# Performance work log

Hardware: AMD Instinct MI355X
Metric: run time of the kernel (lower is better)

The kernel has to match this reference:

```python
import jax, jax.numpy as jnp
import numpy as np

N_LAYER, N_HEAD, N_EMBD, VOCAB, T_CTX, MAXT, B = 6, 8, 128, 18, 30, 2719, 64


def _ln(x, g, b, eps=1e-5):
    m = x.mean(-1, keepdims=True)
    v = ((x - m) ** 2).mean(-1, keepdims=True)
    return (x - m) * jax.lax.rsqrt(v + eps) * g + b


def setup_inputs() -> dict:
    key = jax.random.key(0)
    ks = iter(jax.random.split(key, 64))
    nrm = lambda shape: jax.random.normal(next(ks), shape, jnp.float32) * 0.02
    E, L4 = N_EMBD, 4 * N_EMBD
    inp = dict(
        states=jax.random.normal(next(ks), (B, T_CTX, 4, 84, 84), jnp.float32),
        actions=jax.random.randint(next(ks), (B, T_CTX, 1), 0, VOCAB),
        rtgs=jax.random.normal(next(ks), (B, T_CTX, 1), jnp.float32),
        timesteps=jax.random.randint(next(ks), (B, 1, 1), 0, MAXT),
        conv_w=nrm((E, 4, 84, 84)),
        class_tok=nrm((1, 1, E)),
        in_proj_w=nrm((3 * E, E)), in_proj_b=jnp.zeros(3 * E),
        out_w=nrm((E, E)), out_b=jnp.zeros(E),
        iln1_g=jnp.ones(E), iln1_b=jnp.zeros(E),
        iln2_g=jnp.ones(E), iln2_b=jnp.zeros(E),
        ffn_w1=nrm((E, E)), ffn_b1=jnp.zeros(E),
        ffn_w2=nrm((E, E)), ffn_b2=jnp.zeros(E),
        ret_w=nrm((E, 1)), ret_b=jnp.zeros(E),
        act_table=nrm((VOCAB, E)),
        pos_emb=nrm((1, 3 * T_CTX + 1, E)),
        global_pos_emb=nrm((1, MAXT + 1, E)),
        ln1_g=jnp.ones((N_LAYER, E)), ln1_b=jnp.zeros((N_LAYER, E)),
        Wq=nrm((N_LAYER, E, E)), bq=jnp.zeros((N_LAYER, E)),
        Wk=nrm((N_LAYER, E, E)), bk=jnp.zeros((N_LAYER, E)),
        Wv=nrm((N_LAYER, E, E)), bv=jnp.zeros((N_LAYER, E)),
        Wo=nrm((N_LAYER, E, E)), bo=jnp.zeros((N_LAYER, E)),
        ln2_g=jnp.ones((N_LAYER, E)), ln2_b=jnp.zeros((N_LAYER, E)),
        W1=nrm((N_LAYER, L4, E)), b1=jnp.zeros((N_LAYER, L4)),
        W2=nrm((N_LAYER, E, L4)), b2=jnp.zeros((N_LAYER, E)),
        lnf_g=jnp.ones(E), lnf_b=jnp.zeros(E),
        head_w=nrm((VOCAB, E)),
    )
    return inp


def _forward(states, actions, rtgs, timesteps, conv_w, class_tok, in_proj_w, in_proj_b,
             out_w, out_b, iln1_g, iln1_b, iln2_g, iln2_b, ffn_w1, ffn_b1, ffn_w2, ffn_b2,
             ret_w, ret_b, act_table, pos_emb, global_pos_emb,
             ln1_g, ln1_b, Wq, bq, Wk, bk, Wv, bv, Wo, bo, ln2_g, ln2_b,
             W1, b1, W2, b2, lnf_g, lnf_b, head_w):
    Bsz, T = states.shape[:2]
    E = conv_w.shape[0]
    H, hd = N_HEAD, E // N_HEAD
    # --- inner TIT: patch embed (kernel 84 = frame size -> single patch = one big dot) ---
    obs = states.reshape(Bsz * T, *states.shape[2:])                      # (BT,4,84,84)
    patch = jnp.einsum('bchw,echw->be', obs, conv_w)[:, None, :]          # (BT,1,E)
    x = jnp.concatenate([jnp.broadcast_to(class_tok, (Bsz * T, 1, E)), patch], axis=1)  # (BT,2,E)
    h = _ln(x, iln1_g, iln1_b)
    q, k, v = jnp.split(h @ in_proj_w.T + in_proj_b, 3, axis=-1)
    att = jax.nn.softmax(jnp.einsum('bqe,bke->bqk', q, k) / jnp.sqrt(jnp.float32(E)), axis=-1)
    x = x + jnp.einsum('bqk,bke->bqe', att, v) @ out_w.T + out_b
    h2 = _ln(x, iln2_g, iln2_b)
    x = x + jax.nn.relu(h2 @ ffn_w1.T + ffn_b1) @ ffn_w2.T + ffn_b2
    state_emb = x[:, 0, :].reshape(Bsz, T, E)                             # class token
    # --- token interleave (targets=None path -> length 3T-1, last T-1 actions) ---
    rtg_emb = jnp.tanh(rtgs @ ret_w.T + ret_b)                            # (B,T,E)
    act_emb = jnp.tanh(act_table[actions[..., 0]])                        # (B,T,E)
    Lt = 3 * T - 1
    tok = jnp.zeros((Bsz, Lt, E), states.dtype)
    tok = tok.at[:, 0::3].set(rtg_emb).at[:, 1::3].set(state_emb).at[:, 2::3].set(act_emb[:, 1:])
    pos = global_pos_emb[0][timesteps[:, 0, 0]][:, None, :] + pos_emb[:, :Lt, :]
    x = tok + pos
    # --- outer causal GPT blocks ---
    mask = jnp.tril(jnp.ones((Lt, Lt), bool))
    for i in range(N_LAYER):
        hh = _ln(x, ln1_g[i], ln1_b[i])
        proj = lambda w, b: (hh @ w.T + b).reshape(Bsz, Lt, H, hd).transpose(0, 2, 1, 3)
        q, k, v = proj(Wq[i], bq[i]), proj(Wk[i], bk[i]), proj(Wv[i], bv[i])
        att = jnp.einsum('bhqd,bhkd->bhqk', q, k) / jnp.sqrt(jnp.float32(hd))
        att = jax.nn.softmax(jnp.where(mask, att, -jnp.inf), axis=-1)
        y = jnp.einsum('bhqk,bhkd->bhqd', att, v).transpose(0, 2, 1, 3).reshape(Bsz, Lt, E)
        x = x + y @ Wo[i].T + bo[i]
        hh2 = _ln(x, ln2_g[i], ln2_b[i])
        x = x + jax.nn.gelu(hh2 @ W1[i].T + b1[i], approximate=False) @ W2[i].T + b2[i]
    logits = _ln(x, lnf_g, lnf_b) @ head_w.T
    return logits[:, 1::3, :]                                             # (B,T,vocab) state-position logits


def reference(states, actions, rtgs, timesteps, conv_w, class_tok, in_proj_w, in_proj_b,
              out_w, out_b, iln1_g, iln1_b, iln2_g, iln2_b, ffn_w1, ffn_b1, ffn_w2, ffn_b2,
              ret_w, ret_b, act_table, pos_emb, global_pos_emb,
              ln1_g, ln1_b, Wq, bq, Wk, bk, Wv, bv, Wo, bo, ln2_g, ln2_b,
              W1, b1, W2, b2, lnf_g, lnf_b, head_w):
    return _forward(states, actions, rtgs, timesteps, conv_w, class_tok, in_proj_w, in_proj_b,
                    out_w, out_b, iln1_g, iln1_b, iln2_g, iln2_b, ffn_w1, ffn_b1, ffn_w2, ffn_b2,
                    ret_w, ret_b, act_table, pos_emb, global_pos_emb,
                    ln1_g, ln1_b, Wq, bq, Wk, bk, Wv, bv, Wo, bo, ln2_g, ln2_b,
                    W1, b1, W2, b2, lnf_g, lnf_b, head_w)
```

## Files before the change

### kernel.cpp

```cpp
#include <hip/hip_runtime.h>

#define NB   64
#define NT   30
#define NBT  1920
#define EE   128
#define KP   28224
#define LTK  89
#define NS   5696
#define NLY  6
#define NV   18
#define NZ   21

typedef unsigned short ushort_t;
using bf16x8 = __attribute__((ext_vector_type(8))) short;
using us8    = __attribute__((ext_vector_type(8))) unsigned short;
using f32x4  = __attribute__((ext_vector_type(4))) float;
using f32x16 = __attribute__((ext_vector_type(16))) float;

__device__ inline ushort_t f2bf(float f){
  union { float f; unsigned u; } v; v.f = f;
  unsigned r = v.u + 0x7FFFu + ((v.u >> 16) & 1u);
  return (ushort_t)(r >> 16);
}
__device__ inline float bf2f(ushort_t h){
  union { unsigned u; float f; } v; v.u = ((unsigned)h) << 16; return v.f;
}

__global__ __launch_bounds__(256) void wcvt(
  const float* conv, const float* Wq, const float* Wk, const float* Wv,
  const float* Wo, const float* W1, const float* W2,
  const float* in_w, const float* out_w, const float* f1w, const float* f2w,
  const float* bq, const float* bk, const float* bv,
  ushort_t* dc, ushort_t* dqkv, ushort_t* dout, ushort_t* d1, ushort_t* d2,
  ushort_t* dinw, ushort_t* doutw, ushort_t* df1, ushort_t* df2, float* bqkv)
{
  if (blockIdx.x >= 4776){
    int idx = (blockIdx.x-4776)*256 + threadIdx.x;
    if (idx < NLY*128){ int l=idx>>7, j=idx&127;
      bqkv[l*384+j]=bq[idx]; bqkv[l*384+128+j]=bk[idx]; bqkv[l*384+256+j]=bv[idx]; }
    return;
  }
  long i = 4l*((long)blockIdx.x*256 + threadIdx.x);
  if (i >= 3612672l && i < 3907584l){
    long o = i - 3612672l;
    int  seg = (int)(o / 98304l);
    long off2 = o - (long)seg*98304l;
    long layer = off2 >> 14, rem = off2 & 16383l;
    const float* s = (seg==0) ? Wq : (seg==1) ? Wk : Wv;
    float4 f = *reinterpret_cast<const float4*>(s+off2);
    long dst = layer*49152l + (long)seg*16384l + rem;
    dqkv[dst]=f2bf(f.x); dqkv[dst+1]=f2bf(f.y); dqkv[dst+2]=f2bf(f.z); dqkv[dst+3]=f2bf(f.w);
    return;
  }
  const float* s; ushort_t* d; long off;
  if      (i < 3612672l){ s=conv;  d=dc;    off=i; }
  else if (i < 4005888l){ s=Wo;    d=dout;  off=i-3907584l; }
  else if (i < 4399104l){ s=W1;    d=d1;    off=i-4005888l; }
  else if (i < 4792320l){ s=W2;    d=d2;    off=i-4399104l; }
  else if (i < 4841472l){ s=in_w;  d=dinw;  off=i-4792320l; }
  else if (i < 4857856l){ s=out_w; d=doutw; off=i-4841472l; }
  else if (i < 4874240l){ s=f1w;   d=df1;   off=i-4857856l; }
  else                  { s=f2w;   d=df2;   off=i-4874240l; }
  float4 f = *reinterpret_cast<const float4*>(s+off);
  d[off]=f2bf(f.x); d[off+1]=f2bf(f.y); d[off+2]=f2bf(f.z); d[off+3]=f2bf(f.w);
}

__global__ __launch_bounds__(256) void patch_gemm(
  const float* __restrict__ A, const ushort_t* __restrict__ Wb, float* __restrict__ C)
{
  __shared__ __align__(16) ushort_t As[2][64*64];
  __shared__ __align__(16) ushort_t Ws[2][128*64];
  const int tid = threadIdx.x, lane = tid & 63, wid = tid >> 6;
  const int m0 = blockIdx.x * 64;
  const int kbase = blockIdx.z * 1344;
  float* Cz = C + (size_t)blockIdx.z * NBT * EE;
  const int ra = tid>>2, ca = (tid&3)*16, swa = (ra&7)<<3;
  const int rw = tid>>1, cw = (tid&1)*32, sww = (rw&7)<<3;
  const float*    Ab = A  + (size_t)(m0+ra)*KP + kbase + ca;
  const ushort_t* Wp = Wb + (size_t)rw*KP  + kbase + cw;
  f32x4 acc[8];
  #pragma unroll
  for (int j=0;j<8;j++) acc[j] = (f32x4){0.f,0.f,0.f,0.f};

  auto loadT = [&](float4 (&fa)[4], us8 (&wr)[4], int kt){
    #pragma unroll
    for (int q=0;q<4;q++){
      fa[q] = *reinterpret_cast<const float4*>(Ab + kt*64 + 4*q);
      wr[q] = *reinterpret_cast<const us8*>(Wp + kt*64 + 8*q);
    }
  };
  auto commitT = [&](int buf, const float4 (&fa)[4], const us8 (&wr)[4]){
    us8 o0, o1;
    o0[0]=f2bf(fa[0].x); o0[1]=f2bf(fa[0].y); o0[2]=f2bf(fa[0].z); o0[3]=f2bf(fa[0].w);
    o0[4]=f2bf(fa[1].x); o0[5]=f2bf(fa[1].y); o0[6]=f2bf(fa[1].z); o0[7]=f2bf(fa[1].w);
    o1[0]=f2bf(fa[2].x); o1[1]=f2bf(fa[2].y); o1[2]=f2bf(fa[2].z); o1[3]=f2bf(fa[2].w);
    o1[4]=f2bf(fa[3].x); o1[5]=f2bf(fa[3].y); o1[6]=f2bf(fa[3].z); o1[7]=f2bf(fa[3].w);
    *reinterpret_cast<us8*>(&As[buf][ra*64 + ( ca    ^ swa)]) = o0;
    *reinterpret_cast<us8*>(&As[buf][ra*64 + ((ca+8) ^ swa)]) = o1;
    #pragma unroll
    for (int q=0;q<4;q++)
      *reinterpret_cast<us8*>(&Ws[buf][rw*64 + ((cw+8*q) ^ sww)]) = wr[q];
  };
  auto computeT = [&](int buf){
    #pragma unroll
    for (int ks=0; ks<2; ++ks){
      int arow = wid*16 + (lane&15);
      int kb = ks*32 + (lane>>4)*8;
      bf16x8 a = *reinterpret_cast<const bf16x8*>(&As[buf][arow*64 + (kb ^ ((arow&7)<<3))]);
      #pragma unroll
      for (int nt=0; nt<8; ++nt){
        int nn = nt*16 + (lane&15);
        bf16x8 b = *reinterpret_cast<const bf16x8*>(&Ws[buf][nn*64 + (kb ^ ((nn&7)<<3))]);
        acc[nt] = __builtin_amdgcn_mfma_f32_16x16x32_bf16(a, b, acc[nt], 0,0,0);
      }
    }
  };

  float4 faA[4], faB[4]; us8 wrA[4], wrB[4];
  loadT(faA, wrA, 0);
  loadT(faB, wrB, 1);
  for (int kp = 0; kp < 11; ++kp){
    int kt0 = 2*kp;
    commitT(0, faA, wrA);
    if (kt0 + 2 < 21) loadT(faA, wrA, kt0 + 2);
    __syncthreads();
    computeT(0);
    int kt1 = kt0 + 1;
    if (kt1 < 21){
      commitT(1, faB, wrB);
      if (kt1 + 2 < 21) loadT(faB, wrB, kt1 + 2);
      __syncthreads();
      computeT(1);
    }
  }
  #pragma unroll
  for (int nt=0; nt<8; ++nt)
    #pragma unroll
    for (int rr=0;rr<4;rr++){
      int row = m0 + wid*16 + (lane>>4)*4 + rr;
      int col = nt*16 + (lane&15);
      Cz[row*EE + col] = acc[nt][rr];
    }
}

__global__ __launch_bounds__(256, 2) void inner_tit(
  const float* __restrict__ part, const float* __restrict__ ctok,
  const ushort_t* __restrict__ inw, const float* __restrict__ in_b,
  const ushort_t* __restrict__ outw, const float* __restrict__ out_b,
  const float* __restrict__ g1, const float* __restrict__ b1_,
  const float* __restrict__ g2, const float* __restrict__ b2_,
  const ushort_t* __restrict__ f1wb, const float* __restrict__ fb1,
  const ushort_t* __restrict__ f2wb, const float* __restrict__ fb2,
  const float* __restrict__ rtgs, const int* __restrict__ actions,
  const int* __restrict__ tsteps, const float* __restrict__ ret_w,
  const float* __restrict__ ret_b, const float* __restrict__ act_tab,
  const float* __restrict__ pos_emb, const float* __restrict__ gpos,
  const float* __restrict__ ln1g0, const float* __restrict__ ln1b0,
  float* __restrict__ x, ushort_t* __restrict__ xln)
{
  __shared__ __align__(16) ushort_t wbuf[192*128];
  __shared__ float xs[16*128];
  __shared__ __align__(16) ushort_t hb[16*128];
  __shared__ __align__(16) ushort_t hf[16*128];
  __shared__ __align__(16) ushort_t qkvb[16*400];
  __shared__ float ssm[32];
  const int tid = threadIdx.x, lane = tid & 63, wid = tid >> 6;
  const int bt0 = blockIdx.x * 8;

  auto stageWB = [&](const ushort_t* src, int R){
    for (int c = tid; c < R*16; c += 256){
      int rr = c >> 4, cc = (c & 15) * 8;
      *reinterpret_cast<us8*>(&wbuf[rr*128 + (cc ^ ((rr&7)<<3))]) =
        *reinterpret_cast<const us8*>(src + (size_t)rr*128 + cc);
    }
  };
  auto lnrow = [&](const float* gam, const float* bet, ushort_t* dst){
    int r = tid >> 4, e0 = (tid & 15) * 8;
    float v[8];
    #pragma unroll
    for (int j=0;j<8;j++) v[j] = xs[r*128 + e0 + j];
    float s = 0;
    #pragma unroll
    for (int j=0;j<8;j++) s += v[j];
    s += __shfl_xor(s,1); s += __shfl_xor(s,2); s += __shfl_xor(s,4); s += __shfl_xor(s,8);
    float mean = s * (1.0f/128.0f);
    float vs = 0;
    #pragma unroll
    for (int j=0;j<8;j++){ float d = v[j]-mean; vs += d*d; }
    vs += __shfl_xor(vs,1); vs += __shfl_xor(vs,2); vs += __shfl_xor(vs,4); vs += __shfl_xor(vs,8);
    float rstd = rsqrtf(vs*(1.0f/128.0f) + 1e-5f);
    us8 o;
    #pragma unroll
    for (int j=0;j<8;j++) o[j] = f2bf((v[j]-mean)*rstd*gam[e0+j] + bet[e0+j]);
    *reinterpret_cast<us8*>(&dst[r*128 + (e0 ^ ((r&7)<<3))]) = o;
  };
  auto qgemm = [&](const ushort_t* abuf, int ntg, int rowoff, f32x4& acc){
    int al = lane & 15, kq = (lane>>4)*8;
    int nrow = (ntg*16 + al) - rowoff, nsw = (nrow&7)<<3;
    #pragma unroll
    for (int ks=0; ks<4; ++ks){
      int kb = ks*32 + kq;
      bf16x8 a = *reinterpret_cast<const bf16x8*>(&abuf[al*128 + (kb ^ ((al&7)<<3))]);
      bf16x8 b = *reinterpret_cast<const bf16x8*>(&wbuf[nrow*128 + (kb ^ nsw)]);
      acc = __builtin_amdgcn_mfma_f32_16x16x32_bf16(a, b, acc, 0,0,0);
    }
  };

  { int r = tid >> 4, e0 = (tid & 15) * 8;
    float v[8];
    if ((r & 1) == 0){
      #pragma unroll
      for (int j=0;j<8;j++) v[j] = ctok[e0+j];
    } else {
      #pragma unroll
      for (int j=0;j<8;j++) v[j] = 0.f;
      int bt = bt0 + (r>>1);
      for (int z=0; z<NZ; ++z){
        const float* p = part + (size_t)z*NBT*EE + (size_t)bt*128 + e0;
        float4 f0 = *reinterpret_cast<const float4*>(p);
        float4 f1 = *reinterpret_cast<const float4*>(p+4);
        v[0]+=f0.x; v[1]+=f0.y; v[2]+=f0.z; v[3]+=f0.w;
        v[4]+=f1.x; v[5]+=f1.y; v[6]+=f1.z; v[7]+=f1.w;
      }
    }
    #pragma unroll
    for (int j=0;j<8;j++) xs[r*128 + e0 + j] = v[j];
  }
  stageWB(inw, 192);
  __syncthreads();

  lnrow(g1, b1_, hb);
  __syncthreads();

  { int al = lane & 15;
    #pragma unroll
    for (int j=0;j<3;++j){
      int nt = wid*3 + j;
      f32x4 acc = (f32x4){0.f,0.f,0.f,0.f};
      qgemm(hb, nt, 0, acc);
      float bia = in_b[nt*16 + al];
      #pragma unroll
      for (int rr=0; rr<4; ++rr){
        int row = (lane>>4)*4 + rr;
        qkvb[row*400 + nt*16 + al] = f2bf(acc[rr] + bia);
      }
    }
  }
  __syncthreads();
  stageWB(inw + (size_t)192*128, 192);
  __syncthreads();
  { int al = lane & 15;
    #pragma unroll
    for (int j=0;j<3;++j){
      int nt = 12 + wid*3 + j;
      f32x4 acc = (f32x4){0.f,0.f,0.f,0.f};
      qgemm(hb, nt, 192, acc);
      float bia = in_b[nt*16 + al];
      #pragma unroll
      for (int rr=0; rr<4; ++rr){
        int row = (lane>>4)*4 + rr;
        qkvb[row*400 + nt*16 + al] = f2bf(acc[rr] + bia);
      }
    }
  }
  __syncthreads();

  { int d = tid >> 3, j = tid & 7;
    int i = d >> 2, p = d & 3;
    const ushort_t* qp = &qkvb[(2*i + (p>>1))*400 + j*16];
    const ushort_t* kp = &qkvb[(2*i + (p&1))*400 + 128 + j*16];
    float s = 0;
    #pragma unroll
    for (int e=0;e<16;e++) s += bf2f(qp[e])*bf2f(kp[e]);
    s += __shfl_xor(s,1); s += __shfl_xor(s,2); s += __shfl_xor(s,4);
    if (j == 0) ssm[d] = s;
  }
  stageWB(outw, 128);
  __syncthreads();

  { int r = tid >> 4, e0 = (tid & 15)*8;
    int i = r >> 1, t = r & 1;
    const float sc = 0.08838834764831845f;
    float s0 = ssm[i*4 + t*2]*sc, s1 = ssm[i*4 + t*2 + 1]*sc;
    float m = fmaxf(s0,s1), p0 = __expf(s0-m), p1 = __expf(s1-m);
    float iv = 1.0f/(p0+p1); p0 *= iv; p1 *= iv;
    const ushort_t* v0 = &qkvb[(2*i)*400 + 256 + e0];
    const ushort_t* v1 = &qkvb[(2*i+1)*400 + 256 + e0];
    us8 o;
    #pragma unroll
    for (int j=0;j<8;j++) o[j] = f2bf(p0*bf2f(v0[j]) + p1*bf2f(v1[j]));
    *reinterpret_cast<us8*>(&hb[r*128 + (e0 ^ ((r&7)<<3))]) = o;
  }
  __syncthreads();

  { int al = lane & 15;
    #pragma unroll
    for (int j=0;j<2;++j){
      int nt = wid*2 + j;
      f32x4 acc = (f32x4){0.f,0.f,0.f,0.f};
      qgemm(hb, nt, 0, acc);
      float bia = out_b[nt*16 + al];
      #pragma unroll
      for (int rr=0; rr<4; ++rr){
        int row = (lane>>4)*4 + rr;
        xs[row*128 + nt*16 + al] += acc[rr] + bia;
      }
    }
  }
  __syncthreads();

  lnrow(g2, b2_, hb);
  stageWB(f1wb, 128);
  __syncthreads();

  { int al = lane & 15;
    #pragma unroll
    for (int j=0;j<2;++j){
      int nt = wid*2 + j;
      f32x4 acc = (f32x4){0.f,0.f,0.f,0.f};
      qgemm(hb, nt, 0, acc);
      float bia = fb1[nt*16 + al];
      #pragma unroll
      for (int rr=0; rr<4; ++rr){
        int row = (lane>>4)*4 + rr;
        hf[row*128 + ((nt*16+al) ^ ((row&7)<<3))] = f2bf(fmaxf(acc[rr] + bia, 0.f));
      }
    }
  }
  __syncthreads();

  stageWB(f2wb, 128);
  __syncthreads();
  { int al = lane & 15;
    #pragma unroll
    for (int j=0;j<2;++j){
      int nt = wid*2 + j;
      f32x4 acc = (f32x4){0.f,0.f,0.f,0.f};
      qgemm(hf, nt, 0, acc);
      float bia = fb2[nt*16 + al];
      #pragma unroll
      for (int rr=0; rr<4; ++rr){
        int row = (lane>>4)*4 + rr;
        xs[row*128 + nt*16 + al] += acc[rr] + bia;
      }
    }
  }
  __syncthreads();

  { int q = tid >> 3, j = tid & 7;
    if (q < 24){
      int i = q / 3, kind = q - 3*i;
      int btg = bt0 + i, b = btg / NT, t = btg - b*NT;
      bool valid = !(kind == 2 && t == 0);
      if (valid){
        int prow = (kind==0) ? 3*t : (kind==1) ? 3*t+1 : 3*t-1;
        size_t xrow = ((size_t)b*LTK + prow)*128;
        int ts = tsteps[b];
        int e0 = j*16;
        float v[16];
        if (kind == 1){
          #pragma unroll
          for (int e=0;e<16;e++) v[e] = xs[(2*i)*128 + e0 + e];
        } else if (kind == 0){
          float rv = rtgs[b*NT+t];
          #pragma unroll
          for (int e=0;e<16;e++) v[e] = tanhf(rv*ret_w[e0+e] + ret_b[e0+e]);
        } else {
          int a = actions[b*NT+t];
          #pragma unroll
          for (int e=0;e<16;e++) v[e] = tanhf(act_tab[a*128 + e0 + e]);
        }
        #pragma unroll
        for (int e=0;e<16;e++)
          v[e] += gpos[(size_t)ts*128 + e0 + e] + pos_emb[prow*128 + e0 + e];
        #pragma unroll
        for (int e=0;e<16;e++) x[xrow + e0 + e] = v[e];
        float s = 0;
        #pragma unroll
        for (int e=0;e<16;e++) s += v[e];
        s += __shfl_xor(s,1); s += __shfl_xor(s,2); s += __shfl_xor(s,4);
        float mean = s * (1.0f/128.0f);
        float vs = 0;
        #pragma unroll
        for (int e=0;e<16;e++){ float d = v[e]-mean; vs += d*d; }
        vs += __shfl_xor(vs,1); vs += __shfl_xor(vs,2); vs += __shfl_xor(vs,4);
        float rstd = rsqrtf(vs*(1.0f/128.0f) + 1e-5f);
        #pragma unroll
        for (int e=0;e<16;e++)
          xln[xrow + e0 + e] = f2bf((v[e]-mean)*rstd*ln1g0[e0+e] + ln1b0[e0+e]);
      }
    }
  }
}

__global__ __launch_bounds__(256, 2) void attn_fused(
  const ushort_t* __restrict__ xln, const ushort_t* __restrict__ Wqkv,
  const float* __restrict__ bqkv, ushort_t* __restrict__ y)
{
  __shared__ __align__(16) char sm[69504];
  ushort_t* ab  = (ushort_t*)sm;
  ushort_t* wb  = (ushort_t*)(sm + 24576);
  float*    S   = (float*)sm;
  ushort_t* qa  = (ushort_t*)(sm + 37248);
  ushort_t* ka  = (ushort_t*)(sm + 41472);
  ushort_t* vta = (ushort_t*)(sm + 45696);
  ushort_t* pb  = (ushort_t*)(sm + 49152);
  float*    inv = (float*)(sm + 69120);

  const int b = blockIdx.x >> 3, h = blockIdx.x & 7;
  const int tid = threadIdx.x, lane = tid & 63, wid = tid >> 6;

  for (int idx = tid; idx < 1536; idx += 256){
    int row = idx >> 4, c0 = (idx & 15) * 8;
    us8 v;
    if (row < LTK) v = *reinterpret_cast<const us8*>(xln + ((size_t)(b*LTK+row))*128 + c0);
    else           v = (us8){0,0,0,0,0,0,0,0};
    *reinterpret_cast<us8*>(&ab[row*128 + (c0 ^ ((row&7)<<3))]) = v;
  }
  for (int idx = tid; idx < 384; idx += 256){
    int rr = idx >> 3, c = (idx & 7) * 16;
    int seg = rr >> 4, n = rr & 15;
    const ushort_t* src = Wqkv + (size_t)(seg*128 + h*16 + n)*128 + c;
    int sw = (rr&7)<<3;
    *reinterpret_cast<us8*>(&wb[rr*128 + ( c    ^ sw)]) = *reinterpret_cast<const us8*>(src);
    *reinterpret_cast<us8*>(&wb[rr*128 + ((c+8) ^ sw)]) = *reinterpret_cast<const us8*>(src+8);
  }
  __syncthreads();

  for (int idx = wid; idx < 18; idx += 4){
    int rt = idx / 3, nt = idx - 3*(idx/3);
    f32x4 acc = (f32x4){0.f,0.f,0.f,0.f};
    int arow = rt*16 + (lane&15), asw = (arow&7)<<3;
    int nrow = nt*16 + (lane&15), nsw = (nrow&7)<<3;
    #pragma unroll
    for (int ks=0; ks<4; ++ks){
      int kb = ks*32 + (lane>>4)*8;
      bf16x8 a = *reinterpret_cast<const bf16x8*>(&ab[arow*128 + (kb ^ asw)]);
      bf16x8 bf = *reinterpret_cast<const bf16x8*>(&wb[nrow*128 + (kb ^ nsw)]);
      acc = __builtin_amdgcn_mfma_f32_16x16x32_bf16(a, bf, acc, 0,0,0);
    }
    int d = lane & 15;
    float bia = bqkv[nt*128 + h*16 + d];
    #pragma unroll
    for (int rr=0; rr<4; ++rr){
      int rg = rt*16 + (lane>>4)*4 + rr;
      ushort_t hv = f2bf(acc[rr] + bia);
      if      (nt == 0) qa[rg*22 + d] = hv;
      else if (nt == 1) ka[rg*22 + d] = hv;
      else              vta[d*108 + rg] = hv;
    }
  }
  __syncthreads();

  {
    static const int TR[6] = {0,1,1,2,2,2};
    static const int TC[6] = {0,0,1,0,1,2};
    for (int idx = wid; idx < 6; idx += 4){
      int R = TR[idx], C = TC[idx];
      int arow = R*32 + (lane&31), brow = C*32 + (lane&31);
      int ke = (lane>>5)*8;
      bf16x8 a  = *reinterpret_cast<const bf16x8*>(&qa[arow*22 + ke]);
      bf16x8 bf = *reinterpret_cast<const bf16x8*>(&ka[brow*22 + ke]);
      f32x16 sc = {};
      sc = __builtin_amdgcn_mfma_f32_32x32x16_bf16(a, bf, sc, 0,0,0);
      #pragma unroll
      for (int r=0; r<16; ++r){
        int rin = (r&3) + 8*(r>>2) + 4*(lane>>5);
        S[(R*32+rin)*97 + C*32 + (lane&31)] = sc[r]*0.25f;
      }
    }
  }
  __syncthreads();

  if (tid < 192){
    int t = tid >> 1, half = tid & 1;
    int u0 = half*48;
    float mx = -1e30f;
    if (t < LTK){
      for (int u=u0; u<u0+48; ++u) if (u<=t) mx = fmaxf(mx, S[t*97+u]);
    }
    mx = fmaxf(mx, __shfl_xor(mx,1));
    float smv = 0;
    if (t < LTK){
      for (int u=u0; u<u0+48; ++u){
        float p = 0;
        if (u<=t){ p = __expf(S[t*97+u]-mx); smv += p; }
        pb[t*104+u] = f2bf(p);
      }
    } else {
      for (int u=u0; u<u0+48; ++u) pb[t*104+u] = 0;
    }
    smv += __shfl_xor(smv,1);
    if (half==0) inv[t] = (t<LTK) ? 1.0f/smv : 0.0f;
  }
  __syncthreads();

  for (int rt = wid; rt < 6; rt += 4){
    int arow = rt*16 + (lane&15);
    f32x4 acc = (f32x4){0.f,0.f,0.f,0.f};
    #pragma unroll
    for (int ks=0; ks<3; ++ks){
      int kb = ks*32 + (lane>>4)*8;
      bf16x8 a  = *reinterpret_cast<const bf16x8*>(&pb[arow*104 + kb]);
      bf16x8 bf = *reinterpret_cast<const bf16x8*>(&vta[(lane&15)*108 + kb]);
      acc = __builtin_amdgcn_mfma_f32_16x16x32_bf16(a, bf, acc, 0,0,0);
    }
    #pragma unroll
    for (int rr=0; rr<4; ++rr){
      int rg = rt*16 + (lane>>4)*4 + rr;
      if (rg < LTK)
        y[(size_t)(b*LTK+rg)*128 + h*16 + (lane&15)] = f2bf(acc[rr]*inv[rg]);
    }
  }
}

template<bool HEAD>
__global__ __launch_bounds__(256, 2) void ffn_fused(
  const ushort_t* __restrict__ yg, const ushort_t* __restrict__ Wo,
  const float* __restrict__ bo, const float* __restrict__ g2,
  const float* __restrict__ b2g, const ushort_t* __restrict__ W1,
  const float* __restrict__ b1v, const ushort_t* __restrict__ W2,
  const float* __restrict__ b2v, float* __restrict__ x,
  const float* __restrict__ lnng, const float* __restrict__ lnnb,
  ushort_t* __restrict__ xlnout,
  const float* __restrict__ lnfg, const float* __restrict__ lnfb,
  const float* __restrict__ hw, float* __restrict__ out)
{
  __shared__ __align__(16) char sm[66304];
  ushort_t* wdb = (ushort_t*)sm;
  float*    xr  = (float*)(sm + 32768);
  ushort_t* h2  = (ushort_t*)(sm + 49664);
  ushort_t* f1  = (ushort_t*)(sm + 57856);
  const int tid = threadIdx.x, lane = tid & 63, wid = tid >> 6;
  const int m0 = blockIdx.x * 32;
  const int rr = tid >> 2, qq = tid & 3, swr = (rr&7)<<3;

  auto srcp = [&](int s)->const ushort_t* {
    if (s == 0) return Wo + (size_t)rr*128 + qq*32;
    if (s == 1) return Wo + (size_t)(64+rr)*128 + qq*32;
    int c = (s-2)>>2, r = (s-2)&3;
    if (r == 0) return W1 + (size_t)(c*128+rr)*128 + qq*32;
    if (r == 1) return W1 + (size_t)(c*128+64+rr)*128 + qq*32;
    if (r == 2) return W2 + (size_t)rr*512 + c*128 + qq*32;
    return W2 + (size_t)(64+rr)*512 + c*128 + qq*32;
  };
  auto issue = [&](us8 (&r)[4], int s){
    const ushort_t* p = srcp(s);
    #pragma unroll
    for (int g=0; g<4; ++g) r[g] = *reinterpret_cast<const us8*>(p + 8*g);
  };
  auto commit = [&](int buf, const us8 (&r)[4]){
    ushort_t* d = wdb + buf*8192 + rr*128;
    #pragma unroll
    for (int g=0; g<4; ++g)
      *reinterpret_cast<us8*>(&d[(qq*32+8*g) ^ swr]) = r[g];
  };
  auto gemmT = [&](const ushort_t* abuf, int buf, f32x4* accp){
    int nrow = wid*16 + (lane&15), nsw = (nrow&7)<<3;
    #pragma unroll
    for (int rt=0; rt<2; ++rt){
      int arow = rt*16 + (lane&15), asw = (arow&7)<<3;
      #pragma unroll
      for (int ks=0; ks<4; ++ks){
        int kb = ks*32 + (lane>>4)*8;
        bf16x8 a  = *reinterpret_cast<const bf16x8*>(&abuf[arow*128 + (kb ^ asw)]);
        bf16x8 bb = *reinterpret_cast<const bf16x8*>(&wdb[buf*8192 + nrow*128 + (kb ^ nsw)]);
        accp[rt] = __builtin_amdgcn_mfma_f32_16x16x32_bf16(a, bb, accp[rt], 0,0,0);
      }
    }
  };

  f32x4 accA[2][2], acc2[2][2];
  #pragma unroll
  for (int s_=0;s_<2;++s_){
    accA[s_][0]=(f32x4){0,0,0,0}; accA[s_][1]=(f32x4){0,0,0,0};
    acc2[s_][0]=(f32x4){0,0,0,0}; acc2[s_][1]=(f32x4){0,0,0,0};
  }

  auto computeStage = [&](int k, int buf){
    if (k == 0){
      gemmT(f1, buf, accA[0]);
    } else if (k == 1){
      gemmT(f1, buf, accA[1]);
      #pragma unroll
      for (int s_=0; s_<2; ++s_){
        int col = s_*64 + wid*16 + (lane&15);
        float bia = bo[col];
        #pragma unroll
        for (int rt=0; rt<2; ++rt)
          #pragma unroll
          for (int r4=0; r4<4; ++r4){
            int row = rt*16 + (lane>>4)*4 + r4;
            xr[row*132 + col] = accA[s_][rt][r4] + bia + x[(size_t)(m0+row)*128 + col];
          }
      }
      __syncthreads();
      { int r8 = tid>>3, q8 = tid&7;
        float xv[16];
        #pragma unroll
        for (int i=0;i<16;i++) xv[i] = xr[r8*132 + q8*16 + i];
        float s = 0;
        #pragma unroll
        for (int i=0;i<16;i++) s += xv[i];
        s += __shfl_xor(s,1); s += __shfl_xor(s,2); s += __shfl_xor(s,4);
        float mean = s * (1.0f/128.0f);
        float vs = 0;
        #pragma unroll
        for (int i=0;i<16;i++){ float d = xv[i]-mean; vs += d*d; }
        vs += __shfl_xor(vs,1); vs += __shfl_xor(vs,2); vs += __shfl_xor(vs,4);
        float rstd = rsqrtf(vs*(1.0f/128.0f) + 1e-5f);
        int sw = (r8&7)<<3;
        #pragma unroll
        for (int g=0; g<2; ++g){
          us8 o;
          #pragma unroll
          for (int jj=0;jj<8;jj++){
            int c = q8*16 + g*8 + jj;
            o[jj] = f2bf((xv[g*8+jj]-mean)*rstd*g2[c] + b2g[c]);
          }
          *reinterpret_cast<us8*>(&h2[r8*128 + ((q8*16+g*8) ^ sw)]) = o;
        }
      }
    } else {
      int r = (k-2)&3, c = (k-2)>>2;
      if (r < 2){
        f32x4 ac[2] = {(f32x4){0,0,0,0},(f32x4){0,0,0,0}};
        gemmT(h2, buf, ac);
        int cl = r*64 + wid*16 + (lane&15);
        float bia = b1v[c*128 + cl];
        #pragma unroll
        for (int rt=0; rt<2; ++rt)
          #pragma unroll
          for (int r4=0; r4<4; ++r4){
            int row = rt*16 + (lane>>4)*4 + r4;
            float v = ac[rt][r4] + bia;
            v = 0.5f*v*(1.0f + erff(v*0.70710678118654752f));
            f1[row*128 + (cl ^ ((row&7)<<3))] = f2bf(v);
          }
      } else if (r == 2){
        gemmT(f1, buf, acc2[0]);
      } else {
        gemmT(f1, buf, acc2[1]);
      }
    }
  };

  { int r8 = tid>>3, q8 = tid&7, sw = (r8&7)<<3;
    const ushort_t* src = yg + (size_t)(m0+r8)*128 + q8*16;
    *reinterpret_cast<us8*>(&f1[r8*128 + ((q8*16)   ^ sw)]) = *reinterpret_cast<const us8*>(src);
    *reinterpret_cast<us8*>(&f1[r8*128 + ((q8*16+8) ^ sw)]) = *reinterpret_cast<const us8*>(src+8);
  }
  us8 rA[4], rB[4];
  issue(rA, 0); issue(rB, 1);

  for (int kp = 0; kp < 9; ++kp){
    int k0 = 2*kp, k1 = 2*kp + 1;
    commit(0, rA);
    if (k0 + 2 < 18) issue(rA, k0 + 2);
    __syncthreads();
    computeStage(k0, 0);
    commit(1, rB);
    if (k1 + 2 < 18) issue(rB, k1 + 2);
    __syncthreads();
    computeStage(k1, 1);
  }

  #pragma unroll
  for (int s_=0; s_<2; ++s_){
    int col = s_*64 + wid*16 + (lane&15);
    float bia = b2v[col];
    #pragma unroll
    for (int rt=0; rt<2; ++rt)
      #pragma unroll
      for (int r4=0; r4<4; ++r4){
        int row = rt*16 + (lane>>4)*4 + r4;
        float v = acc2[s_][rt][r4] + bia + xr[row*132 + col];
        xr[row*132 + col] = v;
        if constexpr (!HEAD) x[(size_t)(m0+row)*128 + col] = v;
      }
  }
  __syncthreads();
  if constexpr (!HEAD){
    int r8 = tid>>3, q8 = tid&7;
    float xv[16];
    #pragma unroll
    for (int i=0;i<16;i++) xv[i] = xr[r8*132 + q8*16 + i];
    float s = 0;
    #pragma unroll
    for (int i=0;i<16;i++) s += xv[i];
    s += __shfl_xor(s,1); s += __shfl_xor(s,2); s += __shfl_xor(s,4);
    float mean = s * (1.0f/128.0f);
    float vs = 0;
    #pragma unroll
    for (int i=0;i<16;i++){ float d = xv[i]-mean; vs += d*d; }
    vs += __shfl_xor(vs,1); vs += __shfl_xor(vs,2); vs += __shfl_xor(vs,4);
    float rstd = rsqrtf(vs*(1.0f/128.0f) + 1e-5f);
    #pragma unroll
    for (int g=0; g<2; ++g){
      us8 o;
      #pragma unroll
      for (int jj=0;jj<8;jj++){
        int c = q8*16 + g*8 + jj;
        o[jj] = f2bf((xv[g*8+jj]-mean)*rstd*lnng[c] + lnnb[c]);
      }
      *reinterpret_cast<us8*>(xlnout + (size_t)(m0+r8)*128 + q8*16 + g*8) = o;
    }
  } else {
    for (int r = wid; r < 32; r += 4){
      int s = m0 + r, bb2 = s / LTK, p = s - bb2*LTK;
      if (p % 3 != 1) continue;
      int t = p / 3;
      float v1 = xr[r*132 + lane];
      float v2 = xr[r*132 + 64 + lane];
      float sum = v1 + v2;
      sum += __shfl_xor(sum,1); sum += __shfl_xor(sum,2); sum += __shfl_xor(sum,4);
      sum += __shfl_xor(sum,8); sum += __shfl_xor(sum,16); sum += __shfl_xor(sum,32);
      float mean = sum*(1.0f/128.0f);
      float d1 = v1-mean, d2 = v2-mean;
      float var = d1*d1 + d2*d2;
      var += __shfl_xor(var,1); var += __shfl_xor(var,2); var += __shfl_xor(var,4);
      var += __shfl_xor(var,8); var += __shfl_xor(var,16); var += __shfl_xor(var,32);
      float rstd = rsqrtf(var*(1.0f/128.0f) + 1e-5f);
      float h1 = d1*rstd*lnfg[lane]    + lnfb[lane];
      float h2v= d2*rstd*lnfg[lane+64] + lnfb[lane+64];
      #pragma unroll
      for (int o=0; o<NV; ++o){
        float sdot = h1*hw[o*128+lane] + h2v*hw[o*128+lane+64];
        sdot += __shfl_xor(sdot,1); sdot += __shfl_xor(sdot,2); sdot += __shfl_xor(sdot,4);
        sdot += __shfl_xor(sdot,8); sdot += __shfl_xor(sdot,16); sdot += __shfl_xor(sdot,32);
        if (lane == 0) out[(size_t)(bb2*NT+t)*NV + o] = sdot;
      }
    }
  }
}

extern "C" void kernel_launch(void* const* d_in, const int* in_sizes, int n_in,
                              void* d_out, int out_size, void* d_ws, size_t ws_size,
                              hipStream_t stream)
{
  const float* states  = (const float*)d_in[0];
  const int*   actions = (const int*)  d_in[1];
  const float* rtgs    = (const float*)d_in[2];
  const int*   tsteps  = (const int*)  d_in[3];
  const float* conv_w  = (const float*)d_in[4];
  const float* ctok    = (const float*)d_in[5];
  const float* in_w    = (const float*)d_in[6];
  const float* in_b    = (const float*)d_in[7];
  const float* out_w   = (const float*)d_in[8];
  const float* out_b   = (const float*)d_in[9];
  const float* i1g     = (const float*)d_in[10];
  const float* i1b     = (const float*)d_in[11];
  const float* i2g     = (const float*)d_in[12];
  const float* i2b     = (const float*)d_in[13];
  const float* fw1     = (const float*)d_in[14];
  const float* fb1     = (const float*)d_in[15];
  const float* fw2     = (const float*)d_in[16];
  const float* fb2     = (const float*)d_in[17];
  const float* ret_w   = (const float*)d_in[18];
  const float* ret_b   = (const float*)d_in[19];
  const float* act_tab = (const float*)d_in[20];
  const float* pos_emb = (const float*)d_in[21];
  const float* gpos    = (const float*)d_in[22];
  const float* ln1g    = (const float*)d_in[23];
  const float* ln1b    = (const float*)d_in[24];
  const float* Wq      = (const float*)d_in[25];
  const float* bq      = (const float*)d_in[26];
  const float* Wk      = (const float*)d_in[27];
  const float* bk      = (const float*)d_in[28];
  const float* Wv      = (const float*)d_in[29];
  const float* bv      = (const float*)d_in[30];
  const float* Wo      = (const float*)d_in[31];
  const float* bo      = (const float*)d_in[32];
  const float* ln2g    = (const float*)d_in[33];
  const float* ln2b    = (const float*)d_in[34];
  const float* W1      = (const float*)d_in[35];
  const float* b1      = (const float*)d_in[36];
  const float* W2      = (const float*)d_in[37];
  const float* b2      = (const float*)d_in[38];
  const float* lnfg    = (const float*)d_in[39];
  const float* lnfb    = (const float*)d_in[40];
  const float* head_w  = (const float*)d_in[41];

  char* w = (char*)d_ws;
  size_t off = 0;
  auto alloc = [&](size_t bytes)->char* {
    char* p = w + off; off += (bytes + 255) & ~(size_t)255; return p;
  };
  float*    part  = (float*)   alloc((size_t)NZ*NBT*EE*4);
  float*    x     = (float*)   alloc((size_t)NS*EE*4);
  ushort_t* xlnA  = (ushort_t*)alloc((size_t)NS*EE*2);
  ushort_t* xlnB  = (ushort_t*)alloc((size_t)NS*EE*2);
  ushort_t* yb    = (ushort_t*)alloc((size_t)NS*EE*2);
  ushort_t* cwb   = (ushort_t*)alloc((size_t)EE*KP*2);
  ushort_t* Wqkvb = (ushort_t*)alloc((size_t)NLY*384*128*2);
  ushort_t* Wob   = (ushort_t*)alloc((size_t)NLY*128*128*2);
  ushort_t* W1b   = (ushort_t*)alloc((size_t)NLY*512*128*2);
  ushort_t* W2b   = (ushort_t*)alloc((size_t)NLY*128*512*2);
  ushort_t* inwb  = (ushort_t*)alloc((size_t)384*128*2);
  ushort_t* outwb = (ushort_t*)alloc((size_t)128*128*2);
  ushort_t* f1wb  = (ushort_t*)alloc((size_t)128*128*2);
  ushort_t* f2wb  = (ushort_t*)alloc((size_t)128*128*2);
  float*    bqkv  = (float*)   alloc(NLY*384*4);
  (void)in_sizes; (void)n_in; (void)out_size; (void)ws_size;

  wcvt<<<4779,256,0,stream>>>(conv_w,Wq,Wk,Wv,Wo,W1,W2,
                              in_w,out_w,fw1,fw2, bq,bk,bv,
                              cwb,Wqkvb,Wob,W1b,W2b,
                              inwb,outwb,f1wb,f2wb, bqkv);
  patch_gemm<<<dim3(30,1,NZ),256,0,stream>>>(states, cwb, part);
  inner_tit<<<240,256,0,stream>>>(part, ctok, inwb, in_b, outwb, out_b,
                                  i1g,i1b,i2g,i2b, f1wb,fb1, f2wb,fb2,
                                  rtgs, actions, tsteps, ret_w, ret_b, act_tab,
                                  pos_emb, gpos, ln1g, ln1b, x, xlnA);
  for (int i=0;i<NLY;i++){
    ushort_t* xin  = (i & 1) ? xlnB : xlnA;
    ushort_t* xout = (i & 1) ? xlnA : xlnB;
    attn_fused<<<512,256,0,stream>>>(
      xin, Wqkvb+(size_t)i*49152, bqkv+(size_t)i*384, yb);
    if (i < NLY-1)
      ffn_fused<false><<<178,256,0,stream>>>(
        yb, Wob+(size_t)i*16384, bo+i*128, ln2g+i*128, ln2b+i*128,
        W1b+(size_t)i*65536, b1+i*512, W2b+(size_t)i*65536, b2+i*128, x,
        ln1g+(i+1)*128, ln1b+(i+1)*128, xout,
        nullptr, nullptr, nullptr, nullptr);
    else
      ffn_fused<true><<<178,256,0,stream>>>(
        yb, Wob+(size_t)i*16384, bo+i*128, ln2g+i*128, ln2b+i*128,
        W1b+(size_t)i*65536, b1+i*512, W2b+(size_t)i*65536, b2+i*128, x,
        nullptr, nullptr, nullptr,
        lnfg, lnfb, head_w, (float*)d_out);
  }
}
```

Before: 317.0 us.

## Fuse weight conversion into patch GEMM and convert conv weights on the fly

Merges the weight-conversion kernel and the patch GEMM into one launch. The GEMM blocks now read fp32 conv weights directly and convert them to bf16 while staging into shared memory. The remaining blocks convert the small transformer weights in the same launch. This removes one launch and the separate write-then-read of the bf16 conv weight copy (about 7 MB). In exchange, every M-tile re-reads the fp32 conv weights, each GEMM thread holds more registers, and the conversion work is redone per tile.

```diff
diff --git a/kernel.cpp b/kernel.cpp
--- a/kernel.cpp
+++ b/kernel.cpp
@@ -26,70 +26,72 @@
   union { unsigned u; float f; } v; v.u = ((unsigned)h) << 16; return v.f;
 }
 
-__global__ __launch_bounds__(256) void wcvt(
-  const float* conv, const float* Wq, const float* Wk, const float* Wv,
+__global__ __launch_bounds__(256) void patch_conv(
+  const float* __restrict__ A, const float* __restrict__ convW,
+  const float* Wq, const float* Wk, const float* Wv,
   const float* Wo, const float* W1, const float* W2,
   const float* in_w, const float* out_w, const float* f1w, const float* f2w,
   const float* bq, const float* bk, const float* bv,
-  ushort_t* dc, ushort_t* dqkv, ushort_t* dout, ushort_t* d1, ushort_t* d2,
-  ushort_t* dinw, ushort_t* doutw, ushort_t* df1, ushort_t* df2, float* bqkv)
-{
-  if (blockIdx.x >= 4776){
-    int idx = (blockIdx.x-4776)*256 + threadIdx.x;
-    if (idx < NLY*128){ int l=idx>>7, j=idx&127;
-      bqkv[l*384+j]=bq[idx]; bqkv[l*384+128+j]=bk[idx]; bqkv[l*384+256+j]=bv[idx]; }
-    return;
-  }
-  long i = 4l*((long)blockIdx.x*256 + threadIdx.x);
-  if (i >= 3612672l && i < 3907584l){
-    long o = i - 3612672l;
-    int  seg = (int)(o / 98304l);
-    long off2 = o - (long)seg*98304l;
-    long layer = off2 >> 14, rem = off2 & 16383l;
-    const float* s = (seg==0) ? Wq : (seg==1) ? Wk : Wv;
-    float4 f = *reinterpret_cast<const float4*>(s+off2);
-    long dst = layer*49152l + (long)seg*16384l + rem;
-    dqkv[dst]=f2bf(f.x); dqkv[dst+1]=f2bf(f.y); dqkv[dst+2]=f2bf(f.z); dqkv[dst+3]=f2bf(f.w);
-    return;
-  }
-  const float* s; ushort_t* d; long off;
-  if      (i < 3612672l){ s=conv;  d=dc;    off=i; }
-  else if (i < 4005888l){ s=Wo;    d=dout;  off=i-3907584l; }
-  else if (i < 4399104l){ s=W1;    d=d1;    off=i-4005888l; }
-  else if (i < 4792320l){ s=W2;    d=d2;    off=i-4399104l; }
-  else if (i < 4841472l){ s=in_w;  d=dinw;  off=i-4792320l; }
-  else if (i < 4857856l){ s=out_w; d=doutw; off=i-4841472l; }
-  else if (i < 4874240l){ s=f1w;   d=df1;   off=i-4857856l; }
-  else                  { s=f2w;   d=df2;   off=i-4874240l; }
-  float4 f = *reinterpret_cast<const float4*>(s+off);
-  d[off]=f2bf(f.x); d[off+1]=f2bf(f.y); d[off+2]=f2bf(f.z); d[off+3]=f2bf(f.w);
-}
-
-__global__ __launch_bounds__(256) void patch_gemm(
-  const float* __restrict__ A, const ushort_t* __restrict__ Wb, float* __restrict__ C)
+  ushort_t* dqkv, ushort_t* dout, ushort_t* d1, ushort_t* d2,
+  ushort_t* dinw, ushort_t* doutw, ushort_t* df1, ushort_t* df2,
+  float* bqkv, float* __restrict__ C)
 {
   __shared__ __align__(16) ushort_t As[2][64*64];
   __shared__ __align__(16) ushort_t Ws[2][128*64];
-  const int tid = threadIdx.x, lane = tid & 63, wid = tid >> 6;
-  const int m0 = blockIdx.x * 64;
-  const int kbase = blockIdx.z * 1344;
-  float* Cz = C + (size_t)blockIdx.z * NBT * EE;
+  const int bx = blockIdx.x, tid = threadIdx.x;
+
+  if (bx >= 630){
+    if (bx >= 1878){
+      int idx = (bx-1878)*256 + tid;
+      if (idx < NLY*128){ int l=idx>>7, j=idx&127;
+        bqkv[l*384+j]=bq[idx]; bqkv[l*384+128+j]=bk[idx]; bqkv[l*384+256+j]=bv[idx]; }
+      return;
+    }
+    long i = 4l*((long)(bx-630)*256 + tid) + 3612672l;
+    if (i < 3907584l){
+      long o = i - 3612672l;
+      int  seg = (int)(o / 98304l);
+      long off2 = o - (long)seg*98304l;
+      long layer = off2 >> 14, rem = off2 & 16383l;
+      const float* s = (seg==0) ? Wq : (seg==1) ? Wk : Wv;
+      float4 f = *reinterpret_cast<const float4*>(s+off2);
+      long dst = layer*49152l + (long)seg*16384l + rem;
+      dqkv[dst]=f2bf(f.x); dqkv[dst+1]=f2bf(f.y); dqkv[dst+2]=f2bf(f.z); dqkv[dst+3]=f2bf(f.w);
+      return;
+    }
+    const float* s; ushort_t* d; long off;
+    if      (i < 4005888l){ s=Wo;    d=dout;  off=i-3907584l; }
+    else if (i < 4399104l){ s=W1;    d=d1;    off=i-4005888l; }
+    else if (i < 4792320l){ s=W2;    d=d2;    off=i-4399104l; }
+    else if (i < 4841472l){ s=in_w;  d=dinw;  off=i-4792320l; }
+    else if (i < 4857856l){ s=out_w; d=doutw; off=i-4841472l; }
+    else if (i < 4874240l){ s=f1w;   d=df1;   off=i-4857856l; }
+    else                  { s=f2w;   d=df2;   off=i-4874240l; }
+    float4 f = *reinterpret_cast<const float4*>(s+off);
+    d[off]=f2bf(f.x); d[off+1]=f2bf(f.y); d[off+2]=f2bf(f.z); d[off+3]=f2bf(f.w);
+    return;
+  }
+
+  const int mb = bx / NZ, z = bx - mb*NZ;
+  const int lane = tid & 63, wid = tid >> 6;
+  const int m0 = mb * 64;
+  const int kbase = z * 1344;
+  float* Cz = C + (size_t)z * NBT * EE;
   const int ra = tid>>2, ca = (tid&3)*16, swa = (ra&7)<<3;
   const int rw = tid>>1, cw = (tid&1)*32, sww = (rw&7)<<3;
-  const float*    Ab = A  + (size_t)(m0+ra)*KP + kbase + ca;
-  const ushort_t* Wp = Wb + (size_t)rw*KP  + kbase + cw;
+  const float* Ab = A     + (size_t)(m0+ra)*KP + kbase + ca;
+  const float* Wf = convW + (size_t)rw*KP     + kbase + cw;
   f32x4 acc[8];
   #pragma unroll
   for (int j=0;j<8;j++) acc[j] = (f32x4){0.f,0.f,0.f,0.f};
 
-  auto loadT = [&](float4 (&fa)[4], us8 (&wr)[4], int kt){
-    #pragma unroll
-    for (int q=0;q<4;q++){
-      fa[q] = *reinterpret_cast<const float4*>(Ab + kt*64 + 4*q);
-      wr[q] = *reinterpret_cast<const us8*>(Wp + kt*64 + 8*q);
-    }
-  };
-  auto commitT = [&](int buf, const float4 (&fa)[4], const us8 (&wr)[4]){
+  auto loadT = [&](float4 (&fa)[4], float4 (&wf)[8], int kt){
+    #pragma unroll
+    for (int q=0;q<4;q++) fa[q] = *reinterpret_cast<const float4*>(Ab + kt*64 + 4*q);
+    #pragma unroll
+    for (int q=0;q<8;q++) wf[q] = *reinterpret_cast<const float4*>(Wf + kt*64 + 4*q);
+  };
+  auto commitT = [&](int buf, const float4 (&fa)[4], const float4 (&wf)[8]){
     us8 o0, o1;
     o0[0]=f2bf(fa[0].x); o0[1]=f2bf(fa[0].y); o0[2]=f2bf(fa[0].z); o0[3]=f2bf(fa[0].w);
     o0[4]=f2bf(fa[1].x); o0[5]=f2bf(fa[1].y); o0[6]=f2bf(fa[1].z); o0[7]=f2bf(fa[1].w);
@@ -98,8 +100,13 @@
     *reinterpret_cast<us8*>(&As[buf][ra*64 + ( ca    ^ swa)]) = o0;
     *reinterpret_cast<us8*>(&As[buf][ra*64 + ((ca+8) ^ swa)]) = o1;
     #pragma unroll
-    for (int q=0;q<4;q++)
-      *reinterpret_cast<us8*>(&Ws[buf][rw*64 + ((cw+8*q) ^ sww)]) = wr[q];
+    for (int q=0;q<4;q++){
+      us8 ow;
+      float4 wA = wf[2*q], wB = wf[2*q+1];
+      ow[0]=f2bf(wA.x); ow[1]=f2bf(wA.y); ow[2]=f2bf(wA.z); ow[3]=f2bf(wA.w);
+      ow[4]=f2bf(wB.x); ow[5]=f2bf(wB.y); ow[6]=f2bf(wB.z); ow[7]=f2bf(wB.w);
+      *reinterpret_cast<us8*>(&Ws[buf][rw*64 + ((cw+8*q) ^ sww)]) = ow;
+    }
   };
   auto computeT = [&](int buf){
     #pragma unroll
@@ -116,19 +123,19 @@
     }
   };
 
-  float4 faA[4], faB[4]; us8 wrA[4], wrB[4];
-  loadT(faA, wrA, 0);
-  loadT(faB, wrB, 1);
+  float4 faA[4], faB[4], wfA[8], wfB[8];
+  loadT(faA, wfA, 0);
+  loadT(faB, wfB, 1);
   for (int kp = 0; kp < 11; ++kp){
     int kt0 = 2*kp;
-    commitT(0, faA, wrA);
-    if (kt0 + 2 < 21) loadT(faA, wrA, kt0 + 2);
+    commitT(0, faA, wfA);
+    if (kt0 + 2 < 21) loadT(faA, wfA, kt0 + 2);
     __syncthreads();
     computeT(0);
     int kt1 = kt0 + 1;
     if (kt1 < 21){
-      commitT(1, faB, wrB);
-      if (kt1 + 2 < 21) loadT(faB, wrB, kt1 + 2);
+      commitT(1, faB, wfB);
+      if (kt1 + 2 < 21) loadT(faB, wfB, kt1 + 2);
       __syncthreads();
       computeT(1);
     }
@@ -791,7 +798,6 @@
   ushort_t* xlnA  = (ushort_t*)alloc((size_t)NS*EE*2);
   ushort_t* xlnB  = (ushort_t*)alloc((size_t)NS*EE*2);
   ushort_t* yb    = (ushort_t*)alloc((size_t)NS*EE*2);
-  ushort_t* cwb   = (ushort_t*)alloc((size_t)EE*KP*2);
   ushort_t* Wqkvb = (ushort_t*)alloc((size_t)NLY*384*128*2);
   ushort_t* Wob   = (ushort_t*)alloc((size_t)NLY*128*128*2);
   ushort_t* W1b   = (ushort_t*)alloc((size_t)NLY*512*128*2);
@@ -803,11 +809,10 @@
   float*    bqkv  = (float*)   alloc(NLY*384*4);
   (void)in_sizes; (void)n_in; (void)out_size; (void)ws_size;
 
-  wcvt<<<4779,256,0,stream>>>(conv_w,Wq,Wk,Wv,Wo,W1,W2,
-                              in_w,out_w,fw1,fw2, bq,bk,bv,
-                              cwb,Wqkvb,Wob,W1b,W2b,
-                              inwb,outwb,f1wb,f2wb, bqkv);
-  patch_gemm<<<dim3(30,1,NZ),256,0,stream>>>(states, cwb, part);
+  patch_conv<<<1881,256,0,stream>>>(states, conv_w, Wq,Wk,Wv,Wo,W1,W2,
+                                    in_w,out_w,fw1,fw2, bq,bk,bv,
+                                    Wqkvb,Wob,W1b,W2b, inwb,outwb,f1wb,f2wb,
+                                    bqkv, part);
   inner_tit<<<240,256,0,stream>>>(part, ctok, inwb, in_b, outwb, out_b,
                                   i1g,i1b,i2g,i2b, f1wb,fb1, f2wb,fb2,
                                   rtgs, actions, tsteps, ret_w, ret_b, act_tab,
```

Result: slower. 356.6 us (+12.5%).
